# Kernel optimization log

Hardware: AMD Instinct MI355X
Metric: run time of the kernel (lower is better)

## Reference

```python
import jax, jax.numpy as jnp
import numpy as np

PS = 8          # patch_size
NF = 16         # n_feats
B, H, W = 4, 256, 256
C = NF * PS * PS          # channel_num = 1024
INNER = 3 * C             # heads * channel_num (no head split in source)
SCALE = C ** -0.5         # heads_feats = channel_num
EPS = 1e-5


def _patch(x, shift):
    # reflect-pad then non-overlapping unfold (kernel=PS, stride=PS)
    s = PS // 4
    p = shift * s
    x = jnp.pad(x, ((0, 0), (0, 0), (p, PS - p), (p, PS - p)), mode='reflect')
    b, c, hp, wp = x.shape
    x = x.reshape(b, c, hp // PS, PS, wp // PS, PS)
    # F.unfold ordering: (c, kh, kw) flattened per patch, patches row-major
    x = x.transpose(0, 2, 4, 1, 3, 5).reshape(b, (hp // PS) * (wp // PS), c * PS * PS)
    return x  # [B, N, C*PS*PS]


def _unpatch(x, h, w):
    # inverse of non-overlapping unfold, then crop right/bottom by PS
    b, n, d = x.shape
    c = d // (PS * PS)
    nh, nw = (h + PS) // PS, (w + PS) // PS
    x = x.reshape(b, nh, nw, c, PS, PS).transpose(0, 3, 1, 4, 2, 5)
    x = x.reshape(b, c, nh * PS, nw * PS)
    return x[:, :, :h, :w]


def _ln(x, g, b):
    m = x.mean(-1, keepdims=True)
    v = ((x - m) ** 2).mean(-1, keepdims=True)
    return (x - m) / jnp.sqrt(v + EPS) * g + b


def setup_inputs():
    key = jax.random.key(0)
    ks = jax.random.split(key, 16)
    w = lambda k, shp: jax.random.normal(k, shp, jnp.float32) * 0.02
    return {
        'dr_img': jax.random.normal(ks[0], (B, NF, H, W), jnp.float32),
        'dr_ref': jax.random.normal(ks[1], (B, NF, H, W), jnp.float32),
        'cl_ref': jax.random.normal(ks[2], (B, NF, H, W), jnp.float32),
        'ln_g': jnp.ones((C,), jnp.float32), 'ln_b': jnp.zeros((C,), jnp.float32),
        'Wq': w(ks[3], (C, INNER)), 'bq': jnp.zeros((INNER,), jnp.float32),
        'Wk': w(ks[4], (C, INNER)), 'bk': jnp.zeros((INNER,), jnp.float32),
        'Wv': w(ks[5], (C, INNER)), 'bv': jnp.zeros((INNER,), jnp.float32),
        'Wo': w(ks[6], (INNER, C)), 'bo': jnp.zeros((C,), jnp.float32),
        'ff_ln_g': jnp.ones((C,), jnp.float32), 'ff_ln_b': jnp.zeros((C,), jnp.float32),
        'W1': w(ks[7], (C, C)), 'b1': jnp.zeros((C,), jnp.float32),
        'W2': w(ks[8], (C, C)), 'b2': jnp.zeros((C,), jnp.float32),
    }


def reference(dr_img, dr_ref, cl_ref, ln_g, ln_b, Wq, bq, Wk, bk, Wv, bv,
              Wo, bo, ff_ln_g, ff_ln_b, W1, b1, W2, b2):
    def attn(q, k, v):
        qp = _ln(q, ln_g, ln_b) @ Wq + bq          # [B,N,3C]
        kp = _ln(k, ln_g, ln_b) @ Wk + bk
        vp = _ln(v, ln_g, ln_b) @ Wv + bv
        a = jax.nn.softmax(jnp.einsum('bnd,bmd->bnm', qp, kp) * SCALE, axis=-1)
        return jnp.einsum('bnm,bmd->bnd', a, vp) @ Wo + bo

    def ff(x):
        h = _ln(x, ff_ln_g, ff_ln_b)
        return jax.nn.gelu(h @ W1 + b1, approximate=False) @ W2 + b2

    x = _patch(dr_img, 0)                           # [B,N,C]
    for shift in range(4):
        k = jax.lax.stop_gradient(_patch(dr_ref, shift))
        v = jax.lax.stop_gradient(_patch(cl_ref, shift))
        x = attn(x, k, v) + x
        x = ff(x) + x
    return _unpatch(x, H, W)
```

## Files before the change

kernel.cpp:

```cpp
#include <hip/hip_runtime.h>

typedef unsigned short u16;
typedef float f32x4 __attribute__((ext_vector_type(4)));
typedef __bf16 bf16v8 __attribute__((ext_vector_type(8)));
typedef u16 u16x4 __attribute__((ext_vector_type(4)));

#define WAITV(n) asm volatile("s_waitcnt vmcnt(" #n ")" ::: "memory")
#define BAR() asm volatile("s_barrier" ::: "memory")
#define LGKM0() do { asm volatile("s_waitcnt lgkmcnt(0)" ::: "memory"); \
                     __builtin_amdgcn_sched_barrier(0); } while (0)

__device__ __forceinline__ u16 f2bf(float f) {
  union { float f; unsigned int u; } v; v.f = f;
  unsigned int x = v.u;
  x += 0x7fffu + ((x >> 16) & 1u);
  return (u16)(x >> 16);
}

__device__ __forceinline__ int refl(int i, int n) {
  i = (i < 0) ? -i : i;
  return (i >= n) ? (2 * n - 2 - i) : i;
}

__device__ __forceinline__ void gload_lds16(const void* g, void* l) {
  __builtin_amdgcn_global_load_lds(
      (const __attribute__((address_space(1))) void*)g,
      (__attribute__((address_space(3))) void*)l, 16, 0, 0);
}

enum { EPI_BF16_BIAS = 0, EPI_F32 = 1, EPI_BF16 = 2, EPI_F32_RES = 3, EPI_GELU = 4,
       EPI_BF16_BIASROW = 5 };

__device__ __forceinline__ void xcd_remap(int& bx, int& by, int& bz) {
  const int gx = gridDim.x, gy = gridDim.y;
  const int nwg = gx * gy * (int)gridDim.z;
  const int orig = ((int)blockIdx.z * gy + (int)blockIdx.y) * gx + (int)blockIdx.x;
  const int q = nwg >> 3, r = nwg & 7;
  const int xcd = orig & 7, loc = orig >> 3;
  const int swz = (xcd < r ? xcd * (q + 1) : r * (q + 1) + (xcd - r) * q) + loc;
  const int gxy = gx * gy;
  bz = swz / gxy;
  const int rem = swz - bz * gxy;
  by = rem / gx; bx = rem - by * gx;
}

template <int EPI>
__global__ __launch_bounds__(512, 2) void gemm256(
    const u16* __restrict__ A, const u16* __restrict__ Bt, void* __restrict__ Cp,
    const float* __restrict__ bias, int K, int Nld, long sA, long sB, long sC, long sBias)
{
  extern __shared__ __align__(16) u16 smem[];

  const int t = threadIdx.x;
  int bx, by, bz; xcd_remap(bx, by, bz);
  const int m0 = by * 256, n0 = bx * 256;

  const long Kb = (long)K * 2;
  const int sr8 = t >> 3;
  const int schunk = ((t & 7) ^ (sr8 & 7)) * 16;
  const char* Ag = (const char*)(A + (long)bz * sA + (long)m0 * K) + (long)sr8 * Kb + schunk;
  const char* Bg = (const char*)(Bt + (long)bz * sB + (long)n0 * K) + (long)sr8 * Kb + schunk;

  auto SA = [&](int d, int kt, int i0, int i1) {
    const long ko = (long)kt * 128;
    gload_lds16(Ag + (long)i0 * 64 * Kb + ko, &smem[d * 32768 + i0 * 4096 + t * 8]);
    gload_lds16(Ag + (long)i1 * 64 * Kb + ko, &smem[d * 32768 + i1 * 4096 + t * 8]);
  };
  auto SB = [&](int d, int kt, int i0, int i1) {
    const long ko = (long)kt * 128;
    gload_lds16(Bg + (long)i0 * 64 * Kb + ko, &smem[d * 32768 + 16384 + i0 * 4096 + t * 8]);
    gload_lds16(Bg + (long)i1 * 64 * Kb + ko, &smem[d * 32768 + 16384 + i1 * 4096 + t * 8]);
  };

  const int w = t >> 6, lane = t & 63;
  const int wm = (w >> 2) * 128, wn = (w & 3) * 64;
  const int lr = lane & 15, hi = lane >> 4;
  const int rc0 = ((0 * 4 + hi) ^ (lr & 7)) * 8;
  const int rc1 = ((1 * 4 + hi) ^ (lr & 7)) * 8;

  f32x4 acc[8][4];
  const f32x4 vzero = {0.f, 0.f, 0.f, 0.f};
#pragma unroll
  for (int i = 0; i < 8; i++)
#pragma unroll
    for (int j = 0; j < 4; j++) acc[i][j] = vzero;

  const int NT = K >> 6, NI = NT >> 1;

  SA(0, 0, 0, 1); SA(0, 0, 2, 3); SB(0, 0, 0, 1); SB(0, 0, 2, 3);
  SB(1, 1, 0, 2); SB(1, 1, 1, 3); SA(1, 1, 0, 2);
  WAITV(6);
  BAR();

  for (int i = 0; i < NI; i++) {
    const int t0 = 2 * i;
    const bool last = (i == NI - 1);
#pragma unroll
    for (int h = 0; h < 2; h++) {
      const u16* Ad = &smem[h * 32768];
      const u16* Bd = Ad + 16384;
      bf16v8 b8[4][2];
#pragma unroll
      for (int q = 0; q < 4; q++) {
        bf16v8 a8[2][2];
#pragma unroll
        for (int j = 0; j < 2; j++) {
          const int rbase = (wm + (2 * q + j) * 16 + lr) * 64;
          a8[j][0] = *(const bf16v8*)&Ad[rbase + rc0];
          a8[j][1] = *(const bf16v8*)&Ad[rbase + rc1];
        }
        if (q == 0) {
#pragma unroll
          for (int ni = 0; ni < 4; ni++) {
            const int rbase = (wn + ni * 16 + lr) * 64;
            b8[ni][0] = *(const bf16v8*)&Bd[rbase + rc0];
            b8[ni][1] = *(const bf16v8*)&Bd[rbase + rc1];
          }
        }
        if (h == 0) {
          if (q == 0)           SA(1, t0 + 1, 1, 3);
          else if (!last) {
            if (q == 1)         SB(0, t0 + 2, 0, 2);
            else if (q == 2)    SB(0, t0 + 2, 1, 3);
            else                SA(0, t0 + 2, 0, 2);
          }
        } else if (!last) {
          if (q == 0)           SA(0, t0 + 2, 1, 3);
          else if (q == 1)      SB(1, t0 + 3, 0, 2);
          else if (q == 2)      SB(1, t0 + 3, 1, 3);
          else                  SA(1, t0 + 3, 0, 2);
        }
        BAR();
        LGKM0();
        __builtin_amdgcn_s_setprio(1);
#pragma unroll
        for (int j = 0; j < 2; j++)
#pragma unroll
          for (int ni = 0; ni < 4; ni++) {
            acc[2 * q + j][ni] = __builtin_amdgcn_mfma_f32_16x16x32_bf16(a8[j][0], b8[ni][0], acc[2 * q + j][ni], 0, 0, 0);
            acc[2 * q + j][ni] = __builtin_amdgcn_mfma_f32_16x16x32_bf16(a8[j][1], b8[ni][1], acc[2 * q + j][ni], 0, 0, 0);
          }
        __builtin_amdgcn_s_setprio(0);
        if (h == 0 && q == 3) { if (last) { WAITV(0); } else { WAITV(6); } }
        if (h == 1 && q == 3 && !last) { WAITV(6); }
        BAR();
      }
    }
  }

#pragma unroll
  for (int mi = 0; mi < 8; mi++) {
    const int r0 = m0 + wm + mi * 16 + hi * 4;
#pragma unroll
    for (int ni = 0; ni < 4; ni++) {
      const int col = n0 + wn + ni * 16 + lr;
      float bvv = 0.f;
      if constexpr (EPI == EPI_BF16_BIAS) bvv = bias[bz * sBias + col];
#pragma unroll
      for (int j = 0; j < 4; j++) {
        const long idx = (long)(r0 + j) * Nld + col;
        float val = acc[mi][ni][j] + bvv;
        if constexpr (EPI == EPI_BF16_BIASROW) val += bias[r0 + j];
        if constexpr (EPI == EPI_BF16_BIAS || EPI == EPI_BF16 || EPI == EPI_BF16_BIASROW) {
          ((u16*)Cp + (long)bz * sC)[idx] = f2bf(val);
        } else {
          ((float*)Cp + (long)bz * sC)[idx] = val;
        }
      }
    }
  }
}

template <int EPI>
__global__ __launch_bounds__(512, 4) void gemm128(
    const u16* __restrict__ A, const u16* __restrict__ Bt, void* __restrict__ Cp,
    const float* __restrict__ bias, int K, int ldb, int Nld, long sA, long sB, long sC)
{
  extern __shared__ __align__(16) u16 smem[];

  const int t = threadIdx.x;
  int bx, by, bz; xcd_remap(bx, by, bz);
  const int m0 = by * 128, n0 = bx * 128;

  const long Ka = (long)K * 2;
  const long Kb2 = (long)ldb * 2;
  const int sr8 = t >> 3;
  const int schunk = ((t & 7) ^ (sr8 & 7)) * 16;
  const char* Ag = (const char*)(A + (long)bz * sA + (long)m0 * K) + (long)sr8 * Ka + schunk;
  const char* Bg = (const char*)(Bt + (long)bz * sB + (long)n0 * ldb) + (long)sr8 * Kb2 + schunk;

  auto STAGE = [&](int d, int kt) {
    const long ko = (long)kt * 128;
    gload_lds16(Ag + ko,                &smem[d * 16384 + t * 8]);
    gload_lds16(Ag + 64 * Ka + ko,      &smem[d * 16384 + 4096 + t * 8]);
    gload_lds16(Bg + ko,                &smem[d * 16384 + 8192 + t * 8]);
    gload_lds16(Bg + 64 * Kb2 + ko,     &smem[d * 16384 + 12288 + t * 8]);
  };

  const int w = t >> 6, lane = t & 63;
  const int wm = (w >> 2) * 64, wn = (w & 3) * 32;
  const int lr = lane & 15, hi = lane >> 4;
  const int rc0 = ((0 * 4 + hi) ^ (lr & 7)) * 8;
  const int rc1 = ((1 * 4 + hi) ^ (lr & 7)) * 8;

  f32x4 acc[4][2];
  const f32x4 vzero = {0.f, 0.f, 0.f, 0.f};
#pragma unroll
  for (int i = 0; i < 4; i++)
#pragma unroll
    for (int j = 0; j < 2; j++) acc[i][j] = vzero;

  const int NT = K >> 6;
  STAGE(0, 0);
  STAGE(1, 1);

  for (int kt = 0; kt < NT; kt++) {
    const int d = kt & 1;
    if (kt + 1 < NT) { WAITV(4); } else { WAITV(0); }
    BAR();

    const u16* Ad = &smem[d * 16384];
    const u16* Bd = Ad + 8192;
    bf16v8 a8[4][2], b8[2][2];
#pragma unroll
    for (int mi = 0; mi < 4; mi++) {
      const int rbase = (wm + mi * 16 + lr) * 64;
      a8[mi][0] = *(const bf16v8*)&Ad[rbase + rc0];
      a8[mi][1] = *(const bf16v8*)&Ad[rbase + rc1];
    }
#pragma unroll
    for (int ni = 0; ni < 2; ni++) {
      const int rbase = (wn + ni * 16 + lr) * 64;
      b8[ni][0] = *(const bf16v8*)&Bd[rbase + rc0];
      b8[ni][1] = *(const bf16v8*)&Bd[rbase + rc1];
    }
    __builtin_amdgcn_s_setprio(1);
#pragma unroll
    for (int mi = 0; mi < 4; mi++)
#pragma unroll
      for (int ni = 0; ni < 2; ni++) {
        acc[mi][ni] = __builtin_amdgcn_mfma_f32_16x16x32_bf16(a8[mi][0], b8[ni][0], acc[mi][ni], 0, 0, 0);
        acc[mi][ni] = __builtin_amdgcn_mfma_f32_16x16x32_bf16(a8[mi][1], b8[ni][1], acc[mi][ni], 0, 0, 0);
      }
    __builtin_amdgcn_s_setprio(0);
    asm volatile("s_waitcnt lgkmcnt(0)\n\ts_barrier" ::: "memory");
    if (kt + 2 < NT) STAGE(d, kt + 2);
  }

#pragma unroll
  for (int mi = 0; mi < 4; mi++) {
    const int r0 = m0 + wm + mi * 16 + hi * 4;
#pragma unroll
    for (int ni = 0; ni < 2; ni++) {
      const int col = n0 + wn + ni * 16 + lr;
      float bvv = 0.f;
      if constexpr (EPI == EPI_F32_RES || EPI == EPI_GELU) bvv = bias[col];
#pragma unroll
      for (int j = 0; j < 4; j++) {
        const long idx = (long)(r0 + j) * Nld + col;
        const float val = acc[mi][ni][j] + bvv;
        if constexpr (EPI == EPI_F32) {
          ((float*)Cp + (long)bz * sC)[idx] = val;
        } else if constexpr (EPI == EPI_F32_RES) {
          ((float*)Cp + (long)bz * sC)[idx] += val;
        } else if constexpr (EPI == EPI_GELU) {
          const float gv = 0.5f * val * (1.f + erff(val * 0.70710678118654752440f));
          ((u16*)Cp + (long)bz * sC)[idx] = f2bf(gv);
        } else {
          ((u16*)Cp + (long)bz * sC)[idx] = f2bf(val);
        }
      }
    }
  }
}

__global__ __launch_bounds__(256) void ln_kernel(const float* __restrict__ X,
    const float* __restrict__ g, const float* __restrict__ be, u16* __restrict__ Y)
{
  const long row = blockIdx.x;
  const int t = threadIdx.x;
  const float* xr = X + row * 1024;
  f32x4 v = *(const f32x4*)&xr[t * 4];
  float s = v[0] + v[1] + v[2] + v[3];
  float q = v[0]*v[0] + v[1]*v[1] + v[2]*v[2] + v[3]*v[3];
#pragma unroll
  for (int off = 32; off; off >>= 1) { s += __shfl_xor(s, off); q += __shfl_xor(q, off); }
  __shared__ float red[8];
  if ((t & 63) == 0) { red[t >> 6] = s; red[4 + (t >> 6)] = q; }
  __syncthreads();
  s = red[0] + red[1] + red[2] + red[3];
  q = red[4] + red[5] + red[6] + red[7];
  const float mean = s * (1.f / 1024.f);
  const float rstd = rsqrtf(q * (1.f / 1024.f) - mean * mean + 1e-5f);
  f32x4 gv = *(const f32x4*)&g[t * 4];
  f32x4 bv = *(const f32x4*)&be[t * 4];
  u16x4 o;
#pragma unroll
  for (int i = 0; i < 4; i++) o[i] = f2bf((v[i] - mean) * rstd * gv[i] + bv[i]);
  *(u16x4*)&Y[row * 1024 + t * 4] = o;
}

__global__ __launch_bounds__(256) void patch_kernel(const float* __restrict__ img,
    float* __restrict__ X, int shift)
{
  const int n = blockIdx.x, b = blockIdx.y, t = threadIdx.x;
  float* xr = X + ((long)b * 1152 + n) * 1024;
  if (n >= 1089) {
    const f32x4 z = {0.f, 0.f, 0.f, 0.f};
    *(f32x4*)&xr[t * 4] = z;
    return;
  }
  const int p = shift * 2;
  const int ph = n / 33, pw = n - ph * 33;
  const int d0 = t * 4;
  const int c = d0 >> 6, kh = (d0 >> 3) & 7, kw0 = d0 & 7;
  const int hh = refl(ph * 8 + kh - p, 256);
  const float* src = img + ((long)(b * 16 + c) * 256 + hh) * 256;
  f32x4 v;
#pragma unroll
  for (int i = 0; i < 4; i++) v[i] = src[refl(pw * 8 + kw0 + i - p, 256)];
  *(f32x4*)&xr[d0] = v;
}

__global__ __launch_bounds__(256) void patch_ln_kernel(const float* __restrict__ img,
    const float* __restrict__ g, const float* __restrict__ be, u16* __restrict__ Y, int shift)
{
  const int n = blockIdx.x, b = blockIdx.y, t = threadIdx.x;
  u16* yr = Y + ((long)b * 1152 + n) * 1024;
  if (n >= 1089) {
    const u16x4 z = {0, 0, 0, 0};
    *(u16x4*)&yr[t * 4] = z;
    return;
  }
  const int p = shift * 2;
  const int ph = n / 33, pw = n - ph * 33;
  const int d0 = t * 4;
  const int c = d0 >> 6, kh = (d0 >> 3) & 7, kw0 = d0 & 7;
  const int hh = refl(ph * 8 + kh - p, 256);
  const float* src = img + ((long)(b * 16 + c) * 256 + hh) * 256;
  float v[4];
#pragma unroll
  for (int i = 0; i < 4; i++) v[i] = src[refl(pw * 8 + kw0 + i - p, 256)];
  float s = v[0] + v[1] + v[2] + v[3];
  float q = v[0]*v[0] + v[1]*v[1] + v[2]*v[2] + v[3]*v[3];
#pragma unroll
  for (int off = 32; off; off >>= 1) { s += __shfl_xor(s, off); q += __shfl_xor(q, off); }
  __shared__ float red[8];
  if ((t & 63) == 0) { red[t >> 6] = s; red[4 + (t >> 6)] = q; }
  __syncthreads();
  s = red[0] + red[1] + red[2] + red[3];
  q = red[4] + red[5] + red[6] + red[7];
  const float mean = s * (1.f / 1024.f);
  const float rstd = rsqrtf(q * (1.f / 1024.f) - mean * mean + 1e-5f);
  u16x4 o;
#pragma unroll
  for (int i = 0; i < 4; i++) o[i] = f2bf((v[i] - mean) * rstd * g[d0 + i] + be[d0 + i]);
  *(u16x4*)&yr[d0] = o;
}

__global__ __launch_bounds__(256) void softmax_kernel(const float* __restrict__ L,
    u16* __restrict__ P)
{
  const int r = blockIdx.x, b = blockIdx.y, t = threadIdx.x;
  const float* Lr = L + ((long)b * 1152 + r) * 1152;
  u16* Pr = P + ((long)b * 1152 + r) * 1152;
  float v[5];
  float mx = -1e30f;
#pragma unroll
  for (int i = 0; i < 5; i++) {
    const int j = t + i * 256;
    v[i] = (j < 1089) ? Lr[j] * 0.03125f : -1e30f;
    mx = fmaxf(mx, v[i]);
  }
#pragma unroll
  for (int off = 32; off; off >>= 1) mx = fmaxf(mx, __shfl_xor(mx, off));
  __shared__ float sm[4];
  if ((t & 63) == 0) sm[t >> 6] = mx;
  __syncthreads();
  mx = fmaxf(fmaxf(sm[0], sm[1]), fmaxf(sm[2], sm[3]));
  float p[5];
  float s = 0.f;
#pragma unroll
  for (int i = 0; i < 5; i++) {
    const int j = t + i * 256;
    p[i] = (j < 1089) ? __expf(v[i] - mx) : 0.f;
    s += p[i];
  }
#pragma unroll
  for (int off = 32; off; off >>= 1) s += __shfl_xor(s, off);
  __shared__ float ss[4];
  if ((t & 63) == 0) ss[t >> 6] = s;
  __syncthreads();
  const float inv = 1.f / (ss[0] + ss[1] + ss[2] + ss[3]);
#pragma unroll
  for (int i = 0; i < 5; i++) {
    const int j = t + i * 256;
    if (j < 1152) Pr[j] = f2bf(p[i] * inv);
  }
}

__global__ __launch_bounds__(256) void wtrans_kernel(const float* __restrict__ W,
    u16* __restrict__ Wt, int K, int N)
{
  __shared__ float tile[32][33];
  const int n0 = blockIdx.x * 32, k0 = blockIdx.y * 32;
  const int tx = threadIdx.x & 31, ty = threadIdx.x >> 5;
#pragma unroll
  for (int i = 0; i < 4; i++)
    tile[ty + 8 * i][tx] = W[(long)(k0 + ty + 8 * i) * N + n0 + tx];
  __syncthreads();
#pragma unroll
  for (int i = 0; i < 4; i++)
    Wt[(long)(n0 + ty + 8 * i) * K + k0 + tx] = f2bf(tile[tx][ty + 8 * i]);
}

__global__ __launch_bounds__(256) void catbias_kernel(const float* __restrict__ a,
    const float* __restrict__ b, const float* __restrict__ c, float* __restrict__ o)
{
  const int i = blockIdx.x * 256 + threadIdx.x;
  o[i] = a[i]; o[3072 + i] = b[i]; o[6144 + i] = c[i];
}

__global__ __launch_bounds__(256) void unpatch_kernel(const float* __restrict__ X,
    float* __restrict__ out)
{
  const int idx = blockIdx.x * 256 + threadIdx.x;
  const int w = (idx & 63) * 4;
  const int h = (idx >> 6) & 255;
  const int c = (idx >> 14) & 15;
  const int b = idx >> 18;
  const int ph = h >> 3, kh = h & 7, pw = w >> 3, kw = w & 7;
  const long row = (long)b * 1152 + ph * 33 + pw;
  const int d = c * 64 + kh * 8 + kw;
  const f32x4 v = *(const f32x4*)&X[row * 1024 + d];
  *(f32x4*)&out[((long)(b * 16 + c) * 256 + h) * 256 + w] = v;
}

extern "C" void kernel_launch(void* const* d_in, const int* in_sizes, int n_in,
                              void* d_out, int out_size, void* d_ws, size_t ws_size,
                              hipStream_t stream)
{
  (void)in_sizes; (void)n_in; (void)out_size; (void)ws_size;
  const float* dr_img = (const float*)d_in[0];
  const float* dr_ref = (const float*)d_in[1];
  const float* cl_ref = (const float*)d_in[2];
  const float* ln_g = (const float*)d_in[3];
  const float* ln_be = (const float*)d_in[4];
  const float* Wq = (const float*)d_in[5];
  const float* bq = (const float*)d_in[6];
  const float* Wk = (const float*)d_in[7];
  const float* bk = (const float*)d_in[8];
  const float* Wv = (const float*)d_in[9];
  const float* bv = (const float*)d_in[10];
  const float* Wo = (const float*)d_in[11];
  const float* bo = (const float*)d_in[12];
  const float* ffg = (const float*)d_in[13];
  const float* ffb = (const float*)d_in[14];
  const float* W1 = (const float*)d_in[15];
  const float* b1 = (const float*)d_in[16];
  const float* W2 = (const float*)d_in[17];
  const float* b2 = (const float*)d_in[18];

  const long R = 1152;
  const long MR = 4 * R;

  char* ws = (char*)d_ws;
  size_t off = 0;
  auto alloc = [&](size_t bytes) -> void* {
    void* pp = ws + off;
    off += (bytes + 255) & ~(size_t)255;
    return pp;
  };
  float* x    = (float*)alloc((size_t)MR * 1024 * 4);
  u16* xkv_ln = (u16*)alloc((size_t)3 * MR * 1024 * 2);
  u16* qkv    = (u16*)alloc((size_t)3 * MR * 3072 * 2);
  float* lgt  = (float*)alloc((size_t)4 * R * R * 4);
  u16* P      = (u16*)alloc((size_t)4 * R * R * 2);
  u16* Wqkv_t = (u16*)alloc((size_t)3 * 3072 * 1024 * 2);
  u16* Wo_t   = (u16*)alloc((size_t)1024 * 3072 * 2);
  u16* W1_t   = (u16*)alloc((size_t)1024 * 1024 * 2);
  u16* W2_t   = (u16*)alloc((size_t)1024 * 1024 * 2);
  float* bcat = (float*)alloc((size_t)3 * 3072 * 4);

  u16* x_ln = xkv_ln;
  u16* v_ln = xkv_ln + (size_t)2 * MR * 1024;
  u16* h    = xkv_ln + (size_t)MR * 1024;
  u16* qp   = qkv;
  u16* kp   = qkv + (size_t)MR * 3072;
  u16* vT   = qkv + (size_t)2 * MR * 3072;
  u16* Wv_t = Wqkv_t + (size_t)2 * 3072 * 1024;

  wtrans_kernel<<<dim3(96, 32), 256, 0, stream>>>(Wq, Wqkv_t, 1024, 3072);
  wtrans_kernel<<<dim3(96, 32), 256, 0, stream>>>(Wk, Wqkv_t + (size_t)3072 * 1024, 1024, 3072);
  wtrans_kernel<<<dim3(96, 32), 256, 0, stream>>>(Wv, Wv_t, 1024, 3072);
  wtrans_kernel<<<dim3(32, 96), 256, 0, stream>>>(Wo, Wo_t, 3072, 1024);
  wtrans_kernel<<<dim3(32, 32), 256, 0, stream>>>(W1, W1_t, 1024, 1024);
  wtrans_kernel<<<dim3(32, 32), 256, 0, stream>>>(W2, W2_t, 1024, 1024);
  catbias_kernel<<<12, 256, 0, stream>>>(bq, bk, bv, bcat);

  patch_kernel<<<dim3(1152, 4), 256, 0, stream>>>(dr_img, x, 0);

  const long sAp = (long)MR * 1024;
  const long sBp = (long)3072 * 1024;
  const long sCp = (long)MR * 3072;
  const long sQb = R * 3072;
  const long sLb = R * R;

  for (int shift = 0; shift < 4; shift++) {
    ln_kernel<<<(int)MR, 256, 0, stream>>>(x, ln_g, ln_be, x_ln);
    patch_ln_kernel<<<dim3(1152, 4), 256, 0, stream>>>(dr_ref, ln_g, ln_be, xkv_ln + sAp, shift);
    patch_ln_kernel<<<dim3(1152, 4), 256, 0, stream>>>(cl_ref, ln_g, ln_be, v_ln, shift);

    gemm256<EPI_BF16_BIAS><<<dim3(12, 18, 2), 512, 131072, stream>>>(
        xkv_ln, Wqkv_t, qkv, bcat, 1024, 3072, sAp, sBp, sCp, 3072);

    gemm256<EPI_BF16_BIASROW><<<dim3(18, 12, 1), 512, 131072, stream>>>(
        Wv_t, v_ln, vT, bv, 1024, (int)MR, 0, 0, 0, 0);

    gemm128<EPI_F32><<<dim3(9, 9, 4), 512, 65536, stream>>>(
        qp, kp, lgt, nullptr, 3072, 3072, 1152, sQb, sQb, sLb);

    softmax_kernel<<<dim3(1152, 4), 256, 0, stream>>>(lgt, P);

    gemm128<EPI_BF16><<<dim3(24, 9, 4), 512, 65536, stream>>>(
        P, vT, qp, nullptr, 1152, (int)MR, 3072, sLb, R, sQb);

    gemm128<EPI_F32_RES><<<dim3(8, 36, 1), 512, 65536, stream>>>(
        qp, Wo_t, x, bo, 3072, 3072, 1024, 0, 0, 0);

    ln_kernel<<<(int)MR, 256, 0, stream>>>(x, ffg, ffb, x_ln);
    gemm128<EPI_GELU><<<dim3(8, 36, 1), 512, 65536, stream>>>(
        x_ln, W1_t, h, b1, 1024, 1024, 1024, 0, 0, 0);
    gemm128<EPI_F32_RES><<<dim3(8, 36, 1), 512, 65536, stream>>>(
        h, W2_t, x, b2, 1024, 1024, 1024, 0, 0, 0);
  }

  unpatch_kernel<<<4096, 256, 0, stream>>>(x, (float*)d_out);
}
```

Baseline: 1.334 ms.

## Merge Q/K/V projection GEMMs into one 256x128-tile kernel with simpler pipeline

Replaces the two 256x256-tile gemm256 launches (Q/K batched, and transposed V) with a single qkv_kernel launch. It uses 256-thread blocks, 256x128 tiles, K-step 32 and double-buffered LDS staging, and picks the Q, K or V problem from the block id. This removes one launch and the tail between launches, and gives more, smaller blocks for better CU occupancy and load balance. In exchange each block reuses less data per tile and the finely interleaved prefetch schedule is dropped. The gemm128 MFMA loop is also reordered to iterate over the k-half outermost.

```diff
diff --git a/kernel.cpp b/kernel.cpp
--- a/kernel.cpp
+++ b/kernel.cpp
@@ -7,8 +7,6 @@
 
 #define WAITV(n) asm volatile("s_waitcnt vmcnt(" #n ")" ::: "memory")
 #define BAR() asm volatile("s_barrier" ::: "memory")
-#define LGKM0() do { asm volatile("s_waitcnt lgkmcnt(0)" ::: "memory"); \
-                     __builtin_amdgcn_sched_barrier(0); } while (0)
 
 __device__ __forceinline__ u16 f2bf(float f) {
   union { float f; unsigned int u; } v; v.f = f;
@@ -28,8 +26,7 @@
       (__attribute__((address_space(3))) void*)l, 16, 0, 0);
 }
 
-enum { EPI_BF16_BIAS = 0, EPI_F32 = 1, EPI_BF16 = 2, EPI_F32_RES = 3, EPI_GELU = 4,
-       EPI_BF16_BIASROW = 5 };
+enum { EPI_BF16_BIAS = 0, EPI_F32 = 1, EPI_BF16 = 2, EPI_F32_RES = 3, EPI_GELU = 4 };
 
 __device__ __forceinline__ void xcd_remap(int& bx, int& by, int& bz) {
   const int gx = gridDim.x, gy = gridDim.y;
@@ -44,39 +41,59 @@
   by = rem / gx; bx = rem - by * gx;
 }
 
-template <int EPI>
-__global__ __launch_bounds__(512, 2) void gemm256(
-    const u16* __restrict__ A, const u16* __restrict__ Bt, void* __restrict__ Cp,
-    const float* __restrict__ bias, int K, int Nld, long sA, long sB, long sC, long sBias)
-{
-  extern __shared__ __align__(16) u16 smem[];
+__global__ __launch_bounds__(256, 2) void qkv_kernel(
+    const u16* __restrict__ ln,
+    const u16* __restrict__ Wt,
+    u16* __restrict__ out,
+    const float* __restrict__ bcat,
+    const float* __restrict__ bv)
+{
+  __shared__ __align__(16) u16 smem[2 * 12288];
 
   const int t = threadIdx.x;
-  int bx, by, bz; xcd_remap(bx, by, bz);
-  const int m0 = by * 256, n0 = bx * 256;
-
-  const long Kb = (long)K * 2;
-  const int sr8 = t >> 3;
-  const int schunk = ((t & 7) ^ (sr8 & 7)) * 16;
-  const char* Ag = (const char*)(A + (long)bz * sA + (long)m0 * K) + (long)sr8 * Kb + schunk;
-  const char* Bg = (const char*)(Bt + (long)bz * sB + (long)n0 * K) + (long)sr8 * Kb + schunk;
-
-  auto SA = [&](int d, int kt, int i0, int i1) {
-    const long ko = (long)kt * 128;
-    gload_lds16(Ag + (long)i0 * 64 * Kb + ko, &smem[d * 32768 + i0 * 4096 + t * 8]);
-    gload_lds16(Ag + (long)i1 * 64 * Kb + ko, &smem[d * 32768 + i1 * 4096 + t * 8]);
+  const int nwg = gridDim.x;
+  const int orig = blockIdx.x;
+  const int q8 = nwg >> 3, r8 = nwg & 7;
+  const int xcd = orig & 7, loc = orig >> 3;
+  const int id = (xcd < r8 ? xcd * (q8 + 1) : r8 * (q8 + 1) + (xcd - r8) * q8) + loc;
+  const int z = id / 432;
+  const int f = id - z * 432;
+
+  int m0, n0, Nld;
+  const u16 *Ab, *Bb;
+  u16* Cb;
+  if (z < 2) {
+    m0 = (f / 24) * 256; n0 = (f % 24) * 128;
+    Ab = ln + (size_t)z * 4608 * 1024 + (long)m0 * 1024;
+    Bb = Wt + (size_t)z * 3072 * 1024 + (long)n0 * 1024;
+    Cb = out + (size_t)z * 4608 * 3072;
+    Nld = 3072;
+  } else {
+    m0 = (f / 36) * 256; n0 = (f % 36) * 128;
+    Ab = Wt + (size_t)2 * 3072 * 1024 + (long)m0 * 1024;
+    Bb = ln + (size_t)2 * 4608 * 1024 + (long)n0 * 1024;
+    Cb = out + (size_t)2 * 4608 * 3072;
+    Nld = 4608;
+  }
+
+  const int srow = t >> 2;
+  const int schunk = ((t & 3) ^ ((srow >> 1) & 3)) * 16;
+  const char* Ag = (const char*)Ab + (long)srow * 2048 + schunk;
+  const char* Bg = (const char*)Bb + (long)srow * 2048 + schunk;
+
+  auto STAGE = [&](int d, int kt) {
+    const long ko = (long)kt * 64;
+#pragma unroll
+    for (int i = 0; i < 4; i++)
+      gload_lds16(Ag + (long)i * 64 * 2048 + ko, &smem[d * 12288 + i * 2048 + t * 8]);
+#pragma unroll
+    for (int i = 0; i < 2; i++)
+      gload_lds16(Bg + (long)i * 64 * 2048 + ko, &smem[d * 12288 + 8192 + i * 2048 + t * 8]);
   };
-  auto SB = [&](int d, int kt, int i0, int i1) {
-    const long ko = (long)kt * 128;
-    gload_lds16(Bg + (long)i0 * 64 * Kb + ko, &smem[d * 32768 + 16384 + i0 * 4096 + t * 8]);
-    gload_lds16(Bg + (long)i1 * 64 * Kb + ko, &smem[d * 32768 + 16384 + i1 * 4096 + t * 8]);
-  };
 
   const int w = t >> 6, lane = t & 63;
-  const int wm = (w >> 2) * 128, wn = (w & 3) * 64;
+  const int wm = (w >> 1) * 128, wn = (w & 1) * 64;
   const int lr = lane & 15, hi = lane >> 4;
-  const int rc0 = ((0 * 4 + hi) ^ (lr & 7)) * 8;
-  const int rc1 = ((1 * 4 + hi) ^ (lr & 7)) * 8;
 
   f32x4 acc[8][4];
   const f32x4 vzero = {0.f, 0.f, 0.f, 0.f};
@@ -85,67 +102,37 @@
 #pragma unroll
     for (int j = 0; j < 4; j++) acc[i][j] = vzero;
 
-  const int NT = K >> 6, NI = NT >> 1;
-
-  SA(0, 0, 0, 1); SA(0, 0, 2, 3); SB(0, 0, 0, 1); SB(0, 0, 2, 3);
-  SB(1, 1, 0, 2); SB(1, 1, 1, 3); SA(1, 1, 0, 2);
-  WAITV(6);
-  BAR();
-
-  for (int i = 0; i < NI; i++) {
-    const int t0 = 2 * i;
-    const bool last = (i == NI - 1);
-#pragma unroll
-    for (int h = 0; h < 2; h++) {
-      const u16* Ad = &smem[h * 32768];
-      const u16* Bd = Ad + 16384;
-      bf16v8 b8[4][2];
-#pragma unroll
-      for (int q = 0; q < 4; q++) {
-        bf16v8 a8[2][2];
-#pragma unroll
-        for (int j = 0; j < 2; j++) {
-          const int rbase = (wm + (2 * q + j) * 16 + lr) * 64;
-          a8[j][0] = *(const bf16v8*)&Ad[rbase + rc0];
-          a8[j][1] = *(const bf16v8*)&Ad[rbase + rc1];
-        }
-        if (q == 0) {
-#pragma unroll
-          for (int ni = 0; ni < 4; ni++) {
-            const int rbase = (wn + ni * 16 + lr) * 64;
-            b8[ni][0] = *(const bf16v8*)&Bd[rbase + rc0];
-            b8[ni][1] = *(const bf16v8*)&Bd[rbase + rc1];
-          }
-        }
-        if (h == 0) {
-          if (q == 0)           SA(1, t0 + 1, 1, 3);
-          else if (!last) {
-            if (q == 1)         SB(0, t0 + 2, 0, 2);
-            else if (q == 2)    SB(0, t0 + 2, 1, 3);
-            else                SA(0, t0 + 2, 0, 2);
-          }
-        } else if (!last) {
-          if (q == 0)           SA(0, t0 + 2, 1, 3);
-          else if (q == 1)      SB(1, t0 + 3, 0, 2);
-          else if (q == 2)      SB(1, t0 + 3, 1, 3);
-          else                  SA(1, t0 + 3, 0, 2);
-        }
-        BAR();
-        LGKM0();
-        __builtin_amdgcn_s_setprio(1);
-#pragma unroll
-        for (int j = 0; j < 2; j++)
-#pragma unroll
-          for (int ni = 0; ni < 4; ni++) {
-            acc[2 * q + j][ni] = __builtin_amdgcn_mfma_f32_16x16x32_bf16(a8[j][0], b8[ni][0], acc[2 * q + j][ni], 0, 0, 0);
-            acc[2 * q + j][ni] = __builtin_amdgcn_mfma_f32_16x16x32_bf16(a8[j][1], b8[ni][1], acc[2 * q + j][ni], 0, 0, 0);
-          }
-        __builtin_amdgcn_s_setprio(0);
-        if (h == 0 && q == 3) { if (last) { WAITV(0); } else { WAITV(6); } }
-        if (h == 1 && q == 3 && !last) { WAITV(6); }
-        BAR();
-      }
+  const int NT = 32;
+  STAGE(0, 0);
+  STAGE(1, 1);
+
+  for (int kt = 0; kt < NT; kt++) {
+    const int d = kt & 1;
+    if (kt + 1 < NT) { WAITV(6); } else { WAITV(0); }
+    BAR();
+
+    const u16* Ad = &smem[d * 12288];
+    const u16* Bd = Ad + 8192;
+    bf16v8 a8[8], b8[4];
+#pragma unroll
+    for (int mi = 0; mi < 8; mi++) {
+      const int r = wm + mi * 16 + lr;
+      a8[mi] = *(const bf16v8*)&Ad[r * 32 + ((hi ^ ((r >> 1) & 3)) << 3)];
     }
+#pragma unroll
+    for (int ni = 0; ni < 4; ni++) {
+      const int r = wn + ni * 16 + lr;
+      b8[ni] = *(const bf16v8*)&Bd[r * 32 + ((hi ^ ((r >> 1) & 3)) << 3)];
+    }
+    __builtin_amdgcn_s_setprio(1);
+#pragma unroll
+    for (int mi = 0; mi < 8; mi++)
+#pragma unroll
+      for (int ni = 0; ni < 4; ni++)
+        acc[mi][ni] = __builtin_amdgcn_mfma_f32_16x16x32_bf16(a8[mi], b8[ni], acc[mi][ni], 0, 0, 0);
+    __builtin_amdgcn_s_setprio(0);
+    asm volatile("s_waitcnt lgkmcnt(0)\n\ts_barrier" ::: "memory");
+    if (kt + 2 < NT) STAGE(d, kt + 2);
   }
 
 #pragma unroll
@@ -154,18 +141,13 @@
 #pragma unroll
     for (int ni = 0; ni < 4; ni++) {
       const int col = n0 + wn + ni * 16 + lr;
-      float bvv = 0.f;
-      if constexpr (EPI == EPI_BF16_BIAS) bvv = bias[bz * sBias + col];
+      float cb = 0.f;
+      if (z < 2) cb = bcat[z * 3072 + col];
 #pragma unroll
       for (int j = 0; j < 4; j++) {
-        const long idx = (long)(r0 + j) * Nld + col;
-        float val = acc[mi][ni][j] + bvv;
-        if constexpr (EPI == EPI_BF16_BIASROW) val += bias[r0 + j];
-        if constexpr (EPI == EPI_BF16_BIAS || EPI == EPI_BF16 || EPI == EPI_BF16_BIASROW) {
-          ((u16*)Cp + (long)bz * sC)[idx] = f2bf(val);
-        } else {
-          ((float*)Cp + (long)bz * sC)[idx] = val;
-        }
+        float val = acc[mi][ni][j] + cb;
+        if (z == 2) val += bv[r0 + j];
+        Cb[(long)(r0 + j) * Nld + col] = f2bf(val);
       }
     }
   }
@@ -236,12 +218,12 @@
     }
     __builtin_amdgcn_s_setprio(1);
 #pragma unroll
-    for (int mi = 0; mi < 4; mi++)
-#pragma unroll
-      for (int ni = 0; ni < 2; ni++) {
-        acc[mi][ni] = __builtin_amdgcn_mfma_f32_16x16x32_bf16(a8[mi][0], b8[ni][0], acc[mi][ni], 0, 0, 0);
-        acc[mi][ni] = __builtin_amdgcn_mfma_f32_16x16x32_bf16(a8[mi][1], b8[ni][1], acc[mi][ni], 0, 0, 0);
-      }
+    for (int ks = 0; ks < 2; ks++)
+#pragma unroll
+      for (int mi = 0; mi < 4; mi++)
+#pragma unroll
+        for (int ni = 0; ni < 2; ni++)
+          acc[mi][ni] = __builtin_amdgcn_mfma_f32_16x16x32_bf16(a8[mi][ks], b8[ni][ks], acc[mi][ni], 0, 0, 0);
     __builtin_amdgcn_s_setprio(0);
     asm volatile("s_waitcnt lgkmcnt(0)\n\ts_barrier" ::: "memory");
     if (kt + 2 < NT) STAGE(d, kt + 2);
@@ -501,8 +483,6 @@
   patch_kernel<<<dim3(1152, 4), 256, 0, stream>>>(dr_img, x, 0);
 
   const long sAp = (long)MR * 1024;
-  const long sBp = (long)3072 * 1024;
-  const long sCp = (long)MR * 3072;
   const long sQb = R * 3072;
   const long sLb = R * R;
 
@@ -511,11 +491,7 @@
     patch_ln_kernel<<<dim3(1152, 4), 256, 0, stream>>>(dr_ref, ln_g, ln_be, xkv_ln + sAp, shift);
     patch_ln_kernel<<<dim3(1152, 4), 256, 0, stream>>>(cl_ref, ln_g, ln_be, v_ln, shift);
 
-    gemm256<EPI_BF16_BIAS><<<dim3(12, 18, 2), 512, 131072, stream>>>(
-        xkv_ln, Wqkv_t, qkv, bcat, 1024, 3072, sAp, sBp, sCp, 3072);
-
-    gemm256<EPI_BF16_BIASROW><<<dim3(18, 12, 1), 512, 131072, stream>>>(
-        Wv_t, v_ln, vT, bv, 1024, (int)MR, 0, 0, 0, 0);
+    qkv_kernel<<<1296, 256, 0, stream>>>(xkv_ln, Wqkv_t, qkv, bcat, bv);
 
     gemm128<EPI_F32><<<dim3(9, 9, 4), 512, 65536, stream>>>(
         qp, kp, lgt, nullptr, 3072, 3072, 1152, sQb, sQb, sLb);
```

Result: slower. 1.512 ms (+13.4%).

## Merge QKV GEMMs and LayerNorms into single launches, split-K output projections

Applied to the files above, without the earlier changes.

The three LayerNorm/patch kernels become one 3-D-grid norm3 kernel. The Q/K GEMM launch and the transposed V GEMM launch become one 648-block qkv256 kernel that selects its sub-problem from the block id. The Wo and W2 residual GEMMs are split into two K halves and accumulate into x with atomicAdd, giving 576 blocks instead of 288 to fill the CUs. The MFMA inner loop is also reordered by k-slice. The aim is to cut launch count and fix under-filled grids, at the cost of atomic traffic, nondeterministic summation order, and a possible double-added bias in the split-K path.

```diff
diff --git a/kernel.cpp b/kernel.cpp
--- a/kernel.cpp
+++ b/kernel.cpp
@@ -28,8 +28,7 @@
       (__attribute__((address_space(3))) void*)l, 16, 0, 0);
 }
 
-enum { EPI_BF16_BIAS = 0, EPI_F32 = 1, EPI_BF16 = 2, EPI_F32_RES = 3, EPI_GELU = 4,
-       EPI_BF16_BIASROW = 5 };
+enum { EPI_BF16_BIAS = 0, EPI_F32 = 1, EPI_BF16 = 2, EPI_F32_RES = 3, EPI_GELU = 4 };
 
 __device__ __forceinline__ void xcd_remap(int& bx, int& by, int& bz) {
   const int gx = gridDim.x, gy = gridDim.y;
@@ -44,22 +43,46 @@
   by = rem / gx; bx = rem - by * gx;
 }
 
-template <int EPI>
-__global__ __launch_bounds__(512, 2) void gemm256(
-    const u16* __restrict__ A, const u16* __restrict__ Bt, void* __restrict__ Cp,
-    const float* __restrict__ bias, int K, int Nld, long sA, long sB, long sC, long sBias)
+__global__ __launch_bounds__(512, 2) void qkv256(
+    const u16* __restrict__ ln3,
+    const u16* __restrict__ Wt3,
+    u16* __restrict__ out3,
+    const float* __restrict__ bcat,
+    const float* __restrict__ bv)
 {
   extern __shared__ __align__(16) u16 smem[];
 
   const int t = threadIdx.x;
-  int bx, by, bz; xcd_remap(bx, by, bz);
-  const int m0 = by * 256, n0 = bx * 256;
-
-  const long Kb = (long)K * 2;
+  const int nwg = gridDim.x;
+  const int orig = blockIdx.x;
+  const int q8 = nwg >> 3, r8 = nwg & 7;
+  const int xcd = orig & 7, loc = orig >> 3;
+  const int id = (xcd < r8 ? xcd * (q8 + 1) : r8 * (q8 + 1) + (xcd - r8) * q8) + loc;
+
+  int z, m0, n0, Nld;
+  const u16 *Ab, *Bb;
+  u16* Cb;
+  if (id < 432) {
+    z = id / 216; const int f = id - z * 216;
+    const int bx = f % 12, by = f / 12;
+    m0 = by * 256; n0 = bx * 256; Nld = 3072;
+    Ab = ln3 + (size_t)z * 4718592 + (long)m0 * 1024;
+    Bb = Wt3 + (size_t)z * 3145728 + (long)n0 * 1024;
+    Cb = out3 + (size_t)z * 14155776;
+  } else {
+    z = 2; const int f = id - 432;
+    const int bx = f % 18, by = f / 18;
+    m0 = by * 256; n0 = bx * 256; Nld = 4608;
+    Ab = Wt3 + (size_t)2 * 3145728 + (long)m0 * 1024;
+    Bb = ln3 + (size_t)2 * 4718592 + (long)n0 * 1024;
+    Cb = out3 + (size_t)2 * 14155776;
+  }
+
+  const long Kb = 2048;
   const int sr8 = t >> 3;
   const int schunk = ((t & 7) ^ (sr8 & 7)) * 16;
-  const char* Ag = (const char*)(A + (long)bz * sA + (long)m0 * K) + (long)sr8 * Kb + schunk;
-  const char* Bg = (const char*)(Bt + (long)bz * sB + (long)n0 * K) + (long)sr8 * Kb + schunk;
+  const char* Ag = (const char*)Ab + (long)sr8 * Kb + schunk;
+  const char* Bg = (const char*)Bb + (long)sr8 * Kb + schunk;
 
   auto SA = [&](int d, int kt, int i0, int i1) {
     const long ko = (long)kt * 128;
@@ -85,7 +108,7 @@
 #pragma unroll
     for (int j = 0; j < 4; j++) acc[i][j] = vzero;
 
-  const int NT = K >> 6, NI = NT >> 1;
+  const int NI = 8;
 
   SA(0, 0, 0, 1); SA(0, 0, 2, 3); SB(0, 0, 0, 1); SB(0, 0, 2, 3);
   SB(1, 1, 0, 2); SB(1, 1, 1, 3); SA(1, 1, 0, 2);
@@ -154,18 +177,13 @@
 #pragma unroll
     for (int ni = 0; ni < 4; ni++) {
       const int col = n0 + wn + ni * 16 + lr;
-      float bvv = 0.f;
-      if constexpr (EPI == EPI_BF16_BIAS) bvv = bias[bz * sBias + col];
+      float cb = 0.f;
+      if (z < 2) cb = bcat[z * 3072 + col];
 #pragma unroll
       for (int j = 0; j < 4; j++) {
-        const long idx = (long)(r0 + j) * Nld + col;
-        float val = acc[mi][ni][j] + bvv;
-        if constexpr (EPI == EPI_BF16_BIASROW) val += bias[r0 + j];
-        if constexpr (EPI == EPI_BF16_BIAS || EPI == EPI_BF16 || EPI == EPI_BF16_BIASROW) {
-          ((u16*)Cp + (long)bz * sC)[idx] = f2bf(val);
-        } else {
-          ((float*)Cp + (long)bz * sC)[idx] = val;
-        }
+        float val = acc[mi][ni][j] + cb;
+        if (z == 2) val += bv[r0 + j];
+        Cb[(long)(r0 + j) * Nld + col] = f2bf(val);
       }
     }
   }
@@ -174,27 +192,31 @@
 template <int EPI>
 __global__ __launch_bounds__(512, 4) void gemm128(
     const u16* __restrict__ A, const u16* __restrict__ Bt, void* __restrict__ Cp,
-    const float* __restrict__ bias, int K, int ldb, int Nld, long sA, long sB, long sC)
+    const float* __restrict__ bias, int K, int lda, int ldb, int Nld, int nb,
+    long sA, long sB, long sC)
 {
   extern __shared__ __align__(16) u16 smem[];
 
   const int t = threadIdx.x;
   int bx, by, bz; xcd_remap(bx, by, bz);
+  const int kz = bz / nb, b = bz - kz * nb;
   const int m0 = by * 128, n0 = bx * 128;
 
-  const long Ka = (long)K * 2;
-  const long Kb2 = (long)ldb * 2;
+  const long La = (long)lda * 2;
+  const long Lb = (long)ldb * 2;
   const int sr8 = t >> 3;
   const int schunk = ((t & 7) ^ (sr8 & 7)) * 16;
-  const char* Ag = (const char*)(A + (long)bz * sA + (long)m0 * K) + (long)sr8 * Ka + schunk;
-  const char* Bg = (const char*)(Bt + (long)bz * sB + (long)n0 * ldb) + (long)sr8 * Kb2 + schunk;
+  const char* Ag = (const char*)(A + (long)b * sA + (long)m0 * lda + (long)kz * K)
+                   + (long)sr8 * La + schunk;
+  const char* Bg = (const char*)(Bt + (long)b * sB + (long)n0 * ldb + (long)kz * K)
+                   + (long)sr8 * Lb + schunk;
 
   auto STAGE = [&](int d, int kt) {
     const long ko = (long)kt * 128;
-    gload_lds16(Ag + ko,                &smem[d * 16384 + t * 8]);
-    gload_lds16(Ag + 64 * Ka + ko,      &smem[d * 16384 + 4096 + t * 8]);
-    gload_lds16(Bg + ko,                &smem[d * 16384 + 8192 + t * 8]);
-    gload_lds16(Bg + 64 * Kb2 + ko,     &smem[d * 16384 + 12288 + t * 8]);
+    gload_lds16(Ag + ko,            &smem[d * 16384 + t * 8]);
+    gload_lds16(Ag + 64 * La + ko,  &smem[d * 16384 + 4096 + t * 8]);
+    gload_lds16(Bg + ko,            &smem[d * 16384 + 8192 + t * 8]);
+    gload_lds16(Bg + 64 * Lb + ko,  &smem[d * 16384 + 12288 + t * 8]);
   };
 
   const int w = t >> 6, lane = t & 63;
@@ -236,12 +258,12 @@
     }
     __builtin_amdgcn_s_setprio(1);
 #pragma unroll
-    for (int mi = 0; mi < 4; mi++)
-#pragma unroll
-      for (int ni = 0; ni < 2; ni++) {
-        acc[mi][ni] = __builtin_amdgcn_mfma_f32_16x16x32_bf16(a8[mi][0], b8[ni][0], acc[mi][ni], 0, 0, 0);
-        acc[mi][ni] = __builtin_amdgcn_mfma_f32_16x16x32_bf16(a8[mi][1], b8[ni][1], acc[mi][ni], 0, 0, 0);
-      }
+    for (int ks = 0; ks < 2; ks++)
+#pragma unroll
+      for (int mi = 0; mi < 4; mi++)
+#pragma unroll
+        for (int ni = 0; ni < 2; ni++)
+          acc[mi][ni] = __builtin_amdgcn_mfma_f32_16x16x32_bf16(a8[mi][ks], b8[ni][ks], acc[mi][ni], 0, 0, 0);
     __builtin_amdgcn_s_setprio(0);
     asm volatile("s_waitcnt lgkmcnt(0)\n\ts_barrier" ::: "memory");
     if (kt + 2 < NT) STAGE(d, kt + 2);
@@ -260,18 +282,63 @@
         const long idx = (long)(r0 + j) * Nld + col;
         const float val = acc[mi][ni][j] + bvv;
         if constexpr (EPI == EPI_F32) {
-          ((float*)Cp + (long)bz * sC)[idx] = val;
+          ((float*)Cp + (long)b * sC)[idx] = val;
         } else if constexpr (EPI == EPI_F32_RES) {
-          ((float*)Cp + (long)bz * sC)[idx] += val;
+          atomicAdd(&((float*)Cp + (long)b * sC)[idx], val);
         } else if constexpr (EPI == EPI_GELU) {
           const float gv = 0.5f * val * (1.f + erff(val * 0.70710678118654752440f));
-          ((u16*)Cp + (long)bz * sC)[idx] = f2bf(gv);
+          ((u16*)Cp + (long)b * sC)[idx] = f2bf(gv);
         } else {
-          ((u16*)Cp + (long)bz * sC)[idx] = f2bf(val);
+          ((u16*)Cp + (long)b * sC)[idx] = f2bf(val);
         }
       }
     }
   }
+}
+
+__global__ __launch_bounds__(256) void norm3_kernel(const float* __restrict__ X,
+    const float* __restrict__ dr_ref, const float* __restrict__ cl_ref,
+    const float* __restrict__ g, const float* __restrict__ be,
+    u16* __restrict__ Y3, int shift)
+{
+  const int n = blockIdx.x, b = blockIdx.y, z = blockIdx.z, t = threadIdx.x;
+  const long row = (long)b * 1152 + n;
+  u16* yr = Y3 + (size_t)z * 4718592 + row * 1024;
+  const int d0 = t * 4;
+  float v[4];
+  if (z == 0) {
+    const f32x4 vv = *(const f32x4*)&X[row * 1024 + d0];
+    v[0] = vv[0]; v[1] = vv[1]; v[2] = vv[2]; v[3] = vv[3];
+  } else {
+    if (n >= 1089) {
+      const u16x4 zz = {0, 0, 0, 0};
+      *(u16x4*)&yr[d0] = zz;
+      return;
+    }
+    const float* img = (z == 1) ? dr_ref : cl_ref;
+    const int p = shift * 2;
+    const int ph = n / 33, pw = n - ph * 33;
+    const int c = d0 >> 6, kh = (d0 >> 3) & 7, kw0 = d0 & 7;
+    const int hh = refl(ph * 8 + kh - p, 256);
+    const float* src = img + ((long)(b * 16 + c) * 256 + hh) * 256;
+#pragma unroll
+    for (int i = 0; i < 4; i++) v[i] = src[refl(pw * 8 + kw0 + i - p, 256)];
+  }
+  float s = v[0] + v[1] + v[2] + v[3];
+  float q = v[0]*v[0] + v[1]*v[1] + v[2]*v[2] + v[3]*v[3];
+#pragma unroll
+  for (int off = 32; off; off >>= 1) { s += __shfl_xor(s, off); q += __shfl_xor(q, off); }
+  __shared__ float red[8];
+  if ((t & 63) == 0) { red[t >> 6] = s; red[4 + (t >> 6)] = q; }
+  __syncthreads();
+  s = red[0] + red[1] + red[2] + red[3];
+  q = red[4] + red[5] + red[6] + red[7];
+  const float mean = s * (1.f / 1024.f);
+  const float rstd = rsqrtf(q * (1.f / 1024.f) - mean * mean + 1e-5f);
+  u16x4 o;
+#pragma unroll
+  for (int i = 0; i < 4; i++) o[i] = f2bf((v[i] - mean) * rstd * g[d0 + i] + be[d0 + i]);
+  *(u16x4*)&yr[d0] = o;
 }
 
 __global__ __launch_bounds__(256) void ln_kernel(const float* __restrict__ X,
@@ -320,42 +387,6 @@
 #pragma unroll
   for (int i = 0; i < 4; i++) v[i] = src[refl(pw * 8 + kw0 + i - p, 256)];
   *(f32x4*)&xr[d0] = v;
-}
-
-__global__ __launch_bounds__(256) void patch_ln_kernel(const float* __restrict__ img,
-    const float* __restrict__ g, const float* __restrict__ be, u16* __restrict__ Y, int shift)
-{
-  const int n = blockIdx.x, b = blockIdx.y, t = threadIdx.x;
-  u16* yr = Y + ((long)b * 1152 + n) * 1024;
-  if (n >= 1089) {
-    const u16x4 z = {0, 0, 0, 0};
-    *(u16x4*)&yr[t * 4] = z;
-    return;
-  }
-  const int p = shift * 2;
-  const int ph = n / 33, pw = n - ph * 33;
-  const int d0 = t * 4;
-  const int c = d0 >> 6, kh = (d0 >> 3) & 7, kw0 = d0 & 7;
-  const int hh = refl(ph * 8 + kh - p, 256);
-  const float* src = img + ((long)(b * 16 + c) * 256 + hh) * 256;
-  float v[4];
-#pragma unroll
-  for (int i = 0; i < 4; i++) v[i] = src[refl(pw * 8 + kw0 + i - p, 256)];
-  float s = v[0] + v[1] + v[2] + v[3];
-  float q = v[0]*v[0] + v[1]*v[1] + v[2]*v[2] + v[3]*v[3];
-#pragma unroll
-  for (int off = 32; off; off >>= 1) { s += __shfl_xor(s, off); q += __shfl_xor(q, off); }
-  __shared__ float red[8];
-  if ((t & 63) == 0) { red[t >> 6] = s; red[4 + (t >> 6)] = q; }
-  __syncthreads();
-  s = red[0] + red[1] + red[2] + red[3];
-  q = red[4] + red[5] + red[6] + red[7];
-  const float mean = s * (1.f / 1024.f);
-  const float rstd = rsqrtf(q * (1.f / 1024.f) - mean * mean + 1e-5f);
-  u16x4 o;
-#pragma unroll
-  for (int i = 0; i < 4; i++) o[i] = f2bf((v[i] - mean) * rstd * g[d0 + i] + be[d0 + i]);
-  *(u16x4*)&yr[d0] = o;
 }
 
 __global__ __launch_bounds__(256) void softmax_kernel(const float* __restrict__ L,
@@ -483,7 +514,6 @@
   float* bcat = (float*)alloc((size_t)3 * 3072 * 4);
 
   u16* x_ln = xkv_ln;
-  u16* v_ln = xkv_ln + (size_t)2 * MR * 1024;
   u16* h    = xkv_ln + (size_t)MR * 1024;
   u16* qp   = qkv;
   u16* kp   = qkv + (size_t)MR * 3072;
@@ -500,39 +530,31 @@
 
   patch_kernel<<<dim3(1152, 4), 256, 0, stream>>>(dr_img, x, 0);
 
-  const long sAp = (long)MR * 1024;
-  const long sBp = (long)3072 * 1024;
-  const long sCp = (long)MR * 3072;
   const long sQb = R * 3072;
   const long sLb = R * R;
 
   for (int shift = 0; shift < 4; shift++) {
-    ln_kernel<<<(int)MR, 256, 0, stream>>>(x, ln_g, ln_be, x_ln);
-    patch_ln_kernel<<<dim3(1152, 4), 256, 0, stream>>>(dr_ref, ln_g, ln_be, xkv_ln + sAp, shift);
-    patch_ln_kernel<<<dim3(1152, 4), 256, 0, stream>>>(cl_ref, ln_g, ln_be, v_ln, shift);
-
-    gemm256<EPI_BF16_BIAS><<<dim3(12, 18, 2), 512, 131072, stream>>>(
-        xkv_ln, Wqkv_t, qkv, bcat, 1024, 3072, sAp, sBp, sCp, 3072);
-
-    gemm256<EPI_BF16_BIASROW><<<dim3(18, 12, 1), 512, 131072, stream>>>(
-        Wv_t, v_ln, vT, bv, 1024, (int)MR, 0, 0, 0, 0);
+    norm3_kernel<<<dim3(1152, 4, 3), 256, 0, stream>>>(
+        x, dr_ref, cl_ref, ln_g, ln_be, xkv_ln, shift);
+
+    qkv256<<<648, 512, 131072, stream>>>(xkv_ln, Wqkv_t, qkv, bcat, bv);
 
     gemm128<EPI_F32><<<dim3(9, 9, 4), 512, 65536, stream>>>(
-        qp, kp, lgt, nullptr, 3072, 3072, 1152, sQb, sQb, sLb);
+        qp, kp, lgt, nullptr, 3072, 3072, 3072, 1152, 4, sQb, sQb, sLb);
 
     softmax_kernel<<<dim3(1152, 4), 256, 0, stream>>>(lgt, P);
 
     gemm128<EPI_BF16><<<dim3(24, 9, 4), 512, 65536, stream>>>(
-        P, vT, qp, nullptr, 1152, (int)MR, 3072, sLb, R, sQb);
-
-    gemm128<EPI_F32_RES><<<dim3(8, 36, 1), 512, 65536, stream>>>(
-        qp, Wo_t, x, bo, 3072, 3072, 1024, 0, 0, 0);
+        P, vT, qp, nullptr, 1152, 1152, 4608, 3072, 4, sLb, R, sQb);
+
+    gemm128<EPI_F32_RES><<<dim3(8, 36, 2), 512, 65536, stream>>>(
+        qp, Wo_t, x, bo, 1536, 3072, 3072, 1024, 1, 0, 0, 0);
 
     ln_kernel<<<(int)MR, 256, 0, stream>>>(x, ffg, ffb, x_ln);
     gemm128<EPI_GELU><<<dim3(8, 36, 1), 512, 65536, stream>>>(
-        x_ln, W1_t, h, b1, 1024, 1024, 1024, 0, 0, 0);
-    gemm128<EPI_F32_RES><<<dim3(8, 36, 1), 512, 65536, stream>>>(
-        h, W2_t, x, b2, 1024, 1024, 1024, 0, 0, 0);
+        x_ln, W1_t, h, b1, 1024, 1024, 1024, 1024, 1, 0, 0, 0);
+    gemm128<EPI_F32_RES><<<dim3(8, 36, 2), 512, 65536, stream>>>(
+        h, W2_t, x, b2, 512, 1024, 1024, 1024, 1, 0, 0, 0);
   }
 
   unpatch_kernel<<<4096, 256, 0, stream>>>(x, (float*)d_out);
```

Result: slower. 1.592 ms (+19.3%).
